# Kernel tuning notes

Hardware: AMD Instinct MI355X
Metric: run time of the kernel (lower is better)

## Reference

```python
import jax, jax.numpy as jnp
import numpy as np

WINDOW = 512
N_GLOBAL = 32


def setup_inputs() -> dict:
    key = jax.random.key(0)
    kq, kk, kv = jax.random.split(key, 3)
    shape = (2, 16, 8192, 64)  # [batch, heads, seq_len, head_dim]
    q = jax.random.normal(kq, shape, dtype=jnp.float32)
    k = jax.random.normal(kk, shape, dtype=jnp.float32)
    v = jax.random.normal(kv, shape, dtype=jnp.float32)
    return {"q": q, "k": k, "v": v}


def _sliding_window_attention(q, k, v):
    # Faithful to the torch loop: for i in range(0, S, W) the window is
    # [max(0, i-W//2), min(S, i+W//2)). For S a multiple of W these windows are
    # contiguous, non-overlapping chunks: chunk0 = [0, W//2), then (n-1) chunks
    # of width W. Concatenated output covers positions [0, S - W//2).
    B, H, S, D = q.shape
    W, G, half = WINDOW, N_GLOBAL, WINDOW // 2
    n = S // W
    scale = 1.0 / (D ** 0.5)

    kg = k[:, :, :G]  # [B,H,G,D] global keys
    vg = v[:, :, :G]

    # --- first chunk: positions [0, half) ---
    q0 = q[:, :, :half]
    kc0 = jnp.concatenate([kg, k[:, :, :half]], axis=2)  # [B,H,G+half,D]
    vc0 = jnp.concatenate([vg, v[:, :, :half]], axis=2)
    s0 = jnp.einsum('bhqd,bhkd->bhqk', q0, kc0) * scale
    o0 = jnp.einsum('bhqk,bhkd->bhqd', jax.nn.softmax(s0, axis=-1), vc0)

    # --- remaining (n-1) chunks of width W: positions [half, S-half) ---
    C = n - 1
    qr = q[:, :, half:S - half].reshape(B, H, C, W, D)
    kr = k[:, :, half:S - half].reshape(B, H, C, W, D)
    vr = v[:, :, half:S - half].reshape(B, H, C, W, D)
    kgb = jnp.broadcast_to(kg[:, :, None], (B, H, C, G, D))
    vgb = jnp.broadcast_to(vg[:, :, None], (B, H, C, G, D))
    kc = jnp.concatenate([kgb, kr], axis=3)  # [B,H,C,G+W,D]
    vc = jnp.concatenate([vgb, vr], axis=3)
    s = jnp.einsum('bhcqd,bhckd->bhcqk', qr, kc) * scale
    o = jnp.einsum('bhcqk,bhckd->bhcqd', jax.nn.softmax(s, axis=-1), vc)
    o = o.reshape(B, H, C * W, D)

    return jnp.concatenate([o0, o], axis=2)  # [B,H,S - W//2,D]


def reference(q, k, v):
    return _sliding_window_attention(q, k, v)
```

## Files before the change

kernel.cpp:

```cpp
#include <hip/hip_runtime.h>
#include <hip/hip_bf16.h>

typedef __bf16 v8bf16 __attribute__((ext_vector_type(8)));
typedef __bf16 v2bf16 __attribute__((ext_vector_type(2)));
typedef float  v4f    __attribute__((ext_vector_type(4)));
typedef unsigned int u32;

#define SEQ     8192
#define DIM     64
#define OUTSEQ  7936
#define WIN     512
#define HALF    256
#define BH      32
#define NCHUNK  15
#define MAXT    17
#define NWG_CH  1920
#define VROWT   40

__device__ __forceinline__ v8bf16 cvt8(v4f a, v4f b) {
    v8bf16 r;
    r[0] = (__bf16)a[0]; r[1] = (__bf16)a[1];
    r[2] = (__bf16)a[2]; r[3] = (__bf16)a[3];
    r[4] = (__bf16)b[0]; r[5] = (__bf16)b[1];
    r[6] = (__bf16)b[2]; r[7] = (__bf16)b[3];
    return r;
}

__device__ __forceinline__ v8bf16 load8bf(const float* __restrict__ p) {
    const v4f a = *(const v4f*)p;
    const v4f b = *(const v4f*)(p + 4);
    return cvt8(a, b);
}

__device__ __forceinline__ u32 pk2(float lo, float hi) {
    v2bf16 p; p[0] = (__bf16)lo; p[1] = (__bf16)hi;
    return __builtin_bit_cast(u32, p);
}

__device__ __forceinline__ int vt_idx(int d, int col) {
    return d * VROWT + (col ^ (((d >> 3) & 3) << 3));
}

__global__ __launch_bounds__(256, 4)
void swa_fwd(const float* __restrict__ qg,
             const float* __restrict__ kg,
             const float* __restrict__ vg,
             float* __restrict__ outg)
{
    __shared__ __align__(16) __bf16 Vt[2][DIM * VROWT];

    const int b = blockIdx.x;
    int bh, qoff, koff, ntiles;
    if (b < NWG_CH) {
        const int x  = b & 7;
        const int j  = b >> 3;
        const int qt = j & 3;
        const int cg = ((j >> 2) << 3) | x;
        bh = cg / NCHUNK;
        const int c = cg - bh * NCHUNK;
        koff = HALF + c * WIN;
        qoff = koff + qt * 128;
        ntiles = MAXT;
    } else {
        const int i = b - NWG_CH;
        bh = i >> 1;
        qoff = (i & 1) * 128;
        koff = 0;
        ntiles = 9;
    }

    const float* qb = qg + (size_t)bh * SEQ * DIM;
    const float* kb = kg + (size_t)bh * SEQ * DIM;
    const float* vb = vg + (size_t)bh * SEQ * DIM;

    const int tid  = threadIdx.x;
    const int wave = tid >> 6;
    const int lane = tid & 63;
    const int l15  = lane & 15;
    const int quad = lane >> 4;

    const int qbase = qoff + wave * 32;
    v8bf16 qf[2][2];
    #pragma unroll
    for (int qs = 0; qs < 2; ++qs) {
        const float* qp = qb + (size_t)(qbase + qs * 16 + l15) * DIM + quad * 8;
        qf[qs][0] = load8bf(qp);
        qf[qs][1] = load8bf(qp + 32);
    }

    const int keyduo = tid >> 4;
    const int dquad  = tid & 15;

    {
        const int tokA = 2 * keyduo;
        const v4f a  = *(const v4f*)(vb + (size_t)tokA * DIM + dquad * 4);
        const v4f b2 = *(const v4f*)(vb + (size_t)(tokA + 1) * DIM + dquad * 4);
        #pragma unroll
        for (int i = 0; i < 4; ++i) {
            v2bf16 pr; pr[0] = (__bf16)a[i]; pr[1] = (__bf16)b2[i];
            *(v2bf16*)(&Vt[0][vt_idx(dquad * 4 + i, 2 * keyduo)]) = pr;
        }
    }
    __syncthreads();

    const float cexp = 0.125f * 1.44269504089f;
    const v4f vzero = {0.f, 0.f, 0.f, 0.f};
    float lsum[2] = {0.f, 0.f};
    v4f oacc[2][4];
    #pragma unroll
    for (int qs = 0; qs < 2; ++qs)
        #pragma unroll
        for (int dt = 0; dt < 4; ++dt) oacc[qs][dt] = vzero;

    const int srcA = ((quad & 1) << 5) + l15;
    const int srcB = srcA + 16;
    const bool hi  = quad >= 2;

    int cur = 0;
    for (int t = 0; t < ntiles; ++t) {
        const int base = (t == 0) ? 0 : koff + (t - 1) * 32;
        const bool have_next = (t + 1 < ntiles);

        v4f sva, svb;
        if (have_next) {
            const int tokA = koff + t * 32 + 2 * keyduo;
            sva = *(const v4f*)(vb + (size_t)tokA * DIM + dquad * 4);
            svb = *(const v4f*)(vb + (size_t)(tokA + 1) * DIM + dquad * 4);
        }

        const float* kp = kb + (size_t)(base + l15) * DIM + quad * 8;
        const v8bf16 k00 = load8bf(kp);
        const v8bf16 k01 = load8bf(kp + 32);
        const v8bf16 k10 = load8bf(kp + 16 * DIM);
        const v8bf16 k11 = load8bf(kp + 16 * DIM + 32);

        const __bf16* vcur = Vt[cur];
        v8bf16 vf[4];
        #pragma unroll
        for (int dt = 0; dt < 4; ++dt)
            vf[dt] = *(const v8bf16*)(&vcur[vt_idx(dt * 16 + l15, quad * 8)]);

        #pragma unroll
        for (int qs = 0; qs < 2; ++qs) {
            const v4f S0 = __builtin_amdgcn_mfma_f32_16x16x32_bf16(k01, qf[qs][1],
                           __builtin_amdgcn_mfma_f32_16x16x32_bf16(k00, qf[qs][0], vzero, 0,0,0), 0,0,0);
            const v4f S1 = __builtin_amdgcn_mfma_f32_16x16x32_bf16(k11, qf[qs][1],
                           __builtin_amdgcn_mfma_f32_16x16x32_bf16(k10, qf[qs][0], vzero, 0,0,0), 0,0,0);

            float e0[4], e1[4];
            #pragma unroll
            for (int rr = 0; rr < 4; ++rr) {
                e0[rr] = __builtin_exp2f(S0[rr] * cexp);
                e1[rr] = __builtin_exp2f(S1[rr] * cexp);
                lsum[qs] += e0[rr] + e1[rr];
            }
            const u32 A0 = pk2(e0[0], e0[1]), B0 = pk2(e0[2], e0[3]);
            const u32 A1 = pk2(e1[0], e1[1]), B1 = pk2(e1[2], e1[3]);

            const u32 t0 = (u32)__shfl((int)A0, srcA, 64), u0 = (u32)__shfl((int)A1, srcA, 64);
            const u32 t1 = (u32)__shfl((int)B0, srcA, 64), u1 = (u32)__shfl((int)B1, srcA, 64);
            const u32 t2 = (u32)__shfl((int)A0, srcB, 64), u2 = (u32)__shfl((int)A1, srcB, 64);
            const u32 t3 = (u32)__shfl((int)B0, srcB, 64), u3 = (u32)__shfl((int)B1, srcB, 64);
            u32 pd[4];
            pd[0] = hi ? u0 : t0;  pd[1] = hi ? u1 : t1;
            pd[2] = hi ? u2 : t2;  pd[3] = hi ? u3 : t3;
            const v8bf16 pf = __builtin_bit_cast(v8bf16, *(const u32(*)[4])pd);

            #pragma unroll
            for (int dt = 0; dt < 4; ++dt)
                oacc[qs][dt] = __builtin_amdgcn_mfma_f32_16x16x32_bf16(vf[dt], pf, oacc[qs][dt], 0,0,0);
        }

        if (have_next) {
            __bf16* vnxt = Vt[cur ^ 1];
            #pragma unroll
            for (int i = 0; i < 4; ++i) {
                v2bf16 pr; pr[0] = (__bf16)sva[i]; pr[1] = (__bf16)svb[i];
                *(v2bf16*)(&vnxt[vt_idx(dquad * 4 + i, 2 * keyduo)]) = pr;
            }
        }
        __syncthreads();
        cur ^= 1;
    }

    #pragma unroll
    for (int qs = 0; qs < 2; ++qs) {
        float l = lsum[qs];
        l += __shfl_xor(l, 16, 64);
        l += __shfl_xor(l, 32, 64);
        const float inv = 1.0f / l;
        float* ob = outg + ((size_t)bh * OUTSEQ + qbase + qs * 16 + l15) * DIM;
        #pragma unroll
        for (int dt = 0; dt < 4; ++dt) {
            v4f rv = oacc[qs][dt];
            rv[0] *= inv; rv[1] *= inv; rv[2] *= inv; rv[3] *= inv;
            *(v4f*)(ob + dt * 16 + quad * 4) = rv;
        }
    }
}

extern "C" void kernel_launch(void* const* d_in, const int* in_sizes, int n_in,
                              void* d_out, int out_size, void* d_ws, size_t ws_size,
                              hipStream_t stream) {
    const float* q = (const float*)d_in[0];
    const float* k = (const float*)d_in[1];
    const float* v = (const float*)d_in[2];
    float* out = (float*)d_out;

    const int n_wg = NWG_CH + BH * 2;
    swa_fwd<<<dim3(n_wg), dim3(256), 0, stream>>>(q, k, v, out);
}
```

Baseline: 297.2 us.

## Switch attention MFMAs to 32x32x16 tiles with permlane32 swap for P

Replaces the 16x16x32 bf16 MFMA tiling with 32x32x16 MFMAs, so each wave computes a 32-query by 32-key score block in one accumulator. The P matrix is rearranged into B-operand layout using v_permlane32_swap instead of eight cross-lane shuffles and selects. Q, K and V fragment loads and the output store layout are restructured to match. The aim is fewer MFMA issues and less shuffle overhead per tile, at the cost of larger accumulators and a layout change whose correctness depends on the swap mapping.

```diff
diff --git a/kernel.cpp b/kernel.cpp
--- a/kernel.cpp
+++ b/kernel.cpp
@@ -4,6 +4,7 @@
 typedef __bf16 v8bf16 __attribute__((ext_vector_type(8)));
 typedef __bf16 v2bf16 __attribute__((ext_vector_type(2)));
 typedef float  v4f    __attribute__((ext_vector_type(4)));
+typedef float  v16f   __attribute__((ext_vector_type(16)));
 typedef unsigned int u32;
 
 #define SEQ     8192
@@ -76,16 +77,15 @@
     const int tid  = threadIdx.x;
     const int wave = tid >> 6;
     const int lane = tid & 63;
-    const int l15  = lane & 15;
-    const int quad = lane >> 4;
-
-    const int qbase = qoff + wave * 32;
-    v8bf16 qf[2][2];
-    #pragma unroll
-    for (int qs = 0; qs < 2; ++qs) {
-        const float* qp = qb + (size_t)(qbase + qs * 16 + l15) * DIM + quad * 8;
-        qf[qs][0] = load8bf(qp);
-        qf[qs][1] = load8bf(qp + 32);
+    const int l31  = lane & 31;
+    const int hi8  = (lane >> 5) * 8;
+
+    const int qrow = qoff + wave * 32 + l31;
+    v8bf16 qf[4];
+    {
+        const float* qp = qb + (size_t)qrow * DIM + hi8;
+        #pragma unroll
+        for (int c = 0; c < 4; ++c) qf[c] = load8bf(qp + c * 16);
     }
 
     const int keyduo = tid >> 4;
@@ -104,17 +104,11 @@
     __syncthreads();
 
     const float cexp = 0.125f * 1.44269504089f;
-    const v4f vzero = {0.f, 0.f, 0.f, 0.f};
-    float lsum[2] = {0.f, 0.f};
-    v4f oacc[2][4];
-    #pragma unroll
-    for (int qs = 0; qs < 2; ++qs)
-        #pragma unroll
-        for (int dt = 0; dt < 4; ++dt) oacc[qs][dt] = vzero;
-
-    const int srcA = ((quad & 1) << 5) + l15;
-    const int srcB = srcA + 16;
-    const bool hi  = quad >= 2;
+    const v16f z16 = {0.f,0.f,0.f,0.f,0.f,0.f,0.f,0.f,
+                      0.f,0.f,0.f,0.f,0.f,0.f,0.f,0.f};
+    float lsum = 0.f;
+    v16f oacc[2];
+    oacc[0] = z16; oacc[1] = z16;
 
     int cur = 0;
     for (int t = 0; t < ntiles; ++t) {
@@ -128,48 +122,49 @@
             svb = *(const v4f*)(vb + (size_t)(tokA + 1) * DIM + dquad * 4);
         }
 
-        const float* kp = kb + (size_t)(base + l15) * DIM + quad * 8;
-        const v8bf16 k00 = load8bf(kp);
-        const v8bf16 k01 = load8bf(kp + 32);
-        const v8bf16 k10 = load8bf(kp + 16 * DIM);
-        const v8bf16 k11 = load8bf(kp + 16 * DIM + 32);
+        v8bf16 kf[4];
+        {
+            const float* kp = kb + (size_t)(base + l31) * DIM + hi8;
+            #pragma unroll
+            for (int c = 0; c < 4; ++c) kf[c] = load8bf(kp + c * 16);
+        }
 
         const __bf16* vcur = Vt[cur];
-        v8bf16 vf[4];
-        #pragma unroll
-        for (int dt = 0; dt < 4; ++dt)
-            vf[dt] = *(const v8bf16*)(&vcur[vt_idx(dt * 16 + l15, quad * 8)]);
-
-        #pragma unroll
-        for (int qs = 0; qs < 2; ++qs) {
-            const v4f S0 = __builtin_amdgcn_mfma_f32_16x16x32_bf16(k01, qf[qs][1],
-                           __builtin_amdgcn_mfma_f32_16x16x32_bf16(k00, qf[qs][0], vzero, 0,0,0), 0,0,0);
-            const v4f S1 = __builtin_amdgcn_mfma_f32_16x16x32_bf16(k11, qf[qs][1],
-                           __builtin_amdgcn_mfma_f32_16x16x32_bf16(k10, qf[qs][0], vzero, 0,0,0), 0,0,0);
-
-            float e0[4], e1[4];
+        v8bf16 vf[2][2];
+        #pragma unroll
+        for (int dt = 0; dt < 2; ++dt)
             #pragma unroll
-            for (int rr = 0; rr < 4; ++rr) {
-                e0[rr] = __builtin_exp2f(S0[rr] * cexp);
-                e1[rr] = __builtin_exp2f(S1[rr] * cexp);
-                lsum[qs] += e0[rr] + e1[rr];
-            }
-            const u32 A0 = pk2(e0[0], e0[1]), B0 = pk2(e0[2], e0[3]);
-            const u32 A1 = pk2(e1[0], e1[1]), B1 = pk2(e1[2], e1[3]);
-
-            const u32 t0 = (u32)__shfl((int)A0, srcA, 64), u0 = (u32)__shfl((int)A1, srcA, 64);
-            const u32 t1 = (u32)__shfl((int)B0, srcA, 64), u1 = (u32)__shfl((int)B1, srcA, 64);
-            const u32 t2 = (u32)__shfl((int)A0, srcB, 64), u2 = (u32)__shfl((int)A1, srcB, 64);
-            const u32 t3 = (u32)__shfl((int)B0, srcB, 64), u3 = (u32)__shfl((int)B1, srcB, 64);
-            u32 pd[4];
-            pd[0] = hi ? u0 : t0;  pd[1] = hi ? u1 : t1;
-            pd[2] = hi ? u2 : t2;  pd[3] = hi ? u3 : t3;
-            const v8bf16 pf = __builtin_bit_cast(v8bf16, *(const u32(*)[4])pd);
-
-            #pragma unroll
-            for (int dt = 0; dt < 4; ++dt)
-                oacc[qs][dt] = __builtin_amdgcn_mfma_f32_16x16x32_bf16(vf[dt], pf, oacc[qs][dt], 0,0,0);
-        }
+            for (int ks = 0; ks < 2; ++ks)
+                vf[dt][ks] = *(const v8bf16*)(&vcur[vt_idx(dt * 32 + l31, ks * 16 + hi8)]);
+
+        v16f s = __builtin_amdgcn_mfma_f32_32x32x16_bf16(kf[0], qf[0], z16, 0,0,0);
+        s = __builtin_amdgcn_mfma_f32_32x32x16_bf16(kf[1], qf[1], s, 0,0,0);
+        s = __builtin_amdgcn_mfma_f32_32x32x16_bf16(kf[2], qf[2], s, 0,0,0);
+        s = __builtin_amdgcn_mfma_f32_32x32x16_bf16(kf[3], qf[3], s, 0,0,0);
+
+        u32 P[8];
+        float lacc = 0.f;
+        #pragma unroll
+        for (int r = 0; r < 16; r += 2) {
+            const float ea = __builtin_exp2f(s[r]     * cexp);
+            const float eb = __builtin_exp2f(s[r + 1] * cexp);
+            lacc += ea + eb;
+            P[r >> 1] = pk2(ea, eb);
+        }
+        lsum += lacc;
+
+        asm volatile("v_permlane32_swap_b32 %0, %1" : "+v"(P[0]), "+v"(P[2]));
+        asm volatile("v_permlane32_swap_b32 %0, %1" : "+v"(P[1]), "+v"(P[3]));
+        asm volatile("v_permlane32_swap_b32 %0, %1" : "+v"(P[4]), "+v"(P[6]));
+        asm volatile("v_permlane32_swap_b32 %0, %1" : "+v"(P[5]), "+v"(P[7]));
+
+        const v8bf16 pf0 = __builtin_bit_cast(v8bf16, *(const u32(*)[4])&P[0]);
+        const v8bf16 pf1 = __builtin_bit_cast(v8bf16, *(const u32(*)[4])&P[4]);
+
+        oacc[0] = __builtin_amdgcn_mfma_f32_32x32x16_bf16(vf[0][0], pf0, oacc[0], 0,0,0);
+        oacc[1] = __builtin_amdgcn_mfma_f32_32x32x16_bf16(vf[1][0], pf0, oacc[1], 0,0,0);
+        oacc[0] = __builtin_amdgcn_mfma_f32_32x32x16_bf16(vf[0][1], pf1, oacc[0], 0,0,0);
+        oacc[1] = __builtin_amdgcn_mfma_f32_32x32x16_bf16(vf[1][1], pf1, oacc[1], 0,0,0);
 
         if (have_next) {
             __bf16* vnxt = Vt[cur ^ 1];
@@ -183,18 +178,19 @@
         cur ^= 1;
     }
 
+    const float l = lsum + __shfl_xor(lsum, 32, 64);
+    const float inv = 1.0f / l;
+    float* ob = outg + ((size_t)bh * OUTSEQ + qrow) * DIM + (lane >> 5) * 4;
     #pragma unroll
-    for (int qs = 0; qs < 2; ++qs) {
-        float l = lsum[qs];
-        l += __shfl_xor(l, 16, 64);
-        l += __shfl_xor(l, 32, 64);
-        const float inv = 1.0f / l;
-        float* ob = outg + ((size_t)bh * OUTSEQ + qbase + qs * 16 + l15) * DIM;
-        #pragma unroll
-        for (int dt = 0; dt < 4; ++dt) {
-            v4f rv = oacc[qs][dt];
-            rv[0] *= inv; rv[1] *= inv; rv[2] *= inv; rv[3] *= inv;
-            *(v4f*)(ob + dt * 16 + quad * 4) = rv;
+    for (int dt = 0; dt < 2; ++dt) {
+        #pragma unroll
+        for (int rg = 0; rg < 4; ++rg) {
+            v4f rv;
+            rv[0] = oacc[dt][rg * 4 + 0] * inv;
+            rv[1] = oacc[dt][rg * 4 + 1] * inv;
+            rv[2] = oacc[dt][rg * 4 + 2] * inv;
+            rv[3] = oacc[dt][rg * 4 + 3] * inv;
+            *(v4f*)(ob + dt * 32 + rg * 8) = rv;
         }
     }
 }
```

Result: no change. 293.9 us (-1.1%).
